# Kernel tuning notes

Measured on AMD Instinct MI355X. Metric: run time of the kernel, lower is better.

The kernel has to match this reference:

```python
import jax, jax.numpy as jnp
import numpy as np

B, T, W, H = 4, 4096, 1024, 8
BW = W // H  # block width


@jax.custom_vjp
def sqrt_bound(x):
    return jnp.sqrt(x)

def _sb_fwd(x):
    return jnp.sqrt(x), x

def _sb_bwd(x, g):
    return (g / jnp.sqrt(jnp.clip(4.0 * x, 1e-6)),)

sqrt_bound.defvjp(_sb_fwd, _sb_bwd)


def block_diag_linear(x, w, b):
    # x: [B,T,W] -> [B,T,H,BW]; w: [H,BW,BW]; b: [H,BW]
    xb = x.reshape(x.shape[0], x.shape[1], H, BW)
    y = jnp.einsum('bthi,hij->bthj', xb, w) + b
    return y.reshape(x.shape)


def setup_inputs() -> dict:
    key = jax.random.key(0)
    k1, k2, k3, k4 = jax.random.split(key, 4)
    x = jax.random.normal(k1, (B, T, W), dtype=jnp.float32)
    segment_pos = jnp.broadcast_to(jnp.arange(T, dtype=jnp.int32)[None, :], (B, T))
    std = 1.0 / np.sqrt(BW)
    w_in = std * jax.random.normal(k2, (H, BW, BW), dtype=jnp.float32)
    b_in = jnp.zeros((H, BW), dtype=jnp.float32)
    w_a = std * jax.random.normal(k3, (H, BW, BW), dtype=jnp.float32)
    b_a = jnp.zeros((H, BW), dtype=jnp.float32)
    # rnn_param_init: a_param = log(u^{-0.5} - 1), u ~ U(min_rad^2+eps, max_rad^2+eps)
    u = jax.random.uniform(k4, (W,), dtype=jnp.float32,
                           minval=0.9 ** 2 + 1e-8, maxval=0.999 ** 2 + 1e-8)
    a_param = jnp.log(jnp.exp(-0.5 * jnp.log(u)) - 1.0)
    return {'x': x, 'segment_pos': segment_pos, 'a_param': a_param,
            'w_in': w_in, 'b_in': b_in, 'w_a': w_a, 'b_a': b_a}


def reference(x, segment_pos, a_param, w_in, b_in, w_a, b_a):
    gate_x = jax.nn.sigmoid(block_diag_linear(x, w_in, b_in))
    gate_a = jax.nn.sigmoid(block_diag_linear(x, w_a, b_a))
    log_a = -8.0 * gate_a * jax.nn.softplus(a_param)  # [B,T,W]
    a = jnp.exp(log_a)
    multiplier = sqrt_bound(1.0 - jnp.exp(2.0 * log_a))
    normed_x = x * gate_x * multiplier
    reset = (segment_pos == 0)  # [B,T] bool
    a_eff = a * (~reset)[..., None].astype(a.dtype)
    # diagonal linear recurrence h_t = a_t * h_{t-1} + x_t via lax.scan over time
    def step(h, inp):
        a_t, x_t = inp
        h = a_t * h + x_t
        return h, h
    xs = (jnp.swapaxes(a_eff, 0, 1), jnp.swapaxes(normed_x, 0, 1))  # [T,B,W]
    h0 = jnp.zeros((x.shape[0], x.shape[2]), dtype=x.dtype)
    _, ys = jax.lax.scan(step, h0, xs)
    return jnp.swapaxes(ys, 0, 1)  # [B,T,W]
```

## Files before the change

### kernel.cpp

```cpp
#include <hip/hip_runtime.h>
#include <math.h>

#define NB 4
#define NT 4096
#define NW 1024
#define NH 8
#define CHUNK 64
#define NCH 64
#define STRIDE_A 136

typedef __attribute__((ext_vector_type(8))) short short8;
typedef __attribute__((ext_vector_type(4))) float f32x4;

__device__ __forceinline__ short bf16rne(float f) {
    unsigned u = __float_as_uint(f);
    u += 0x7fffu + ((u >> 16) & 1u);
    return (short)(u >> 16);
}

__global__ __launch_bounds__(256)
void k0_wfrag(const float* __restrict__ w_in, const float* __restrict__ w_a,
              short* __restrict__ wfH, uint4* __restrict__ poison)
{
    int idx = blockIdx.x * 256 + threadIdx.x;
    uint4 nv; nv.x = nv.y = nv.z = nv.w = 0xFFFFFFFFu;
    poison[idx]          = nv;
    poison[idx + 65536]  = nv;
    poison[idx + 131072] = nv;

    int j4 = (idx & 31) * 4;
    int i  = (idx >> 5) & 127;
    int h  = (idx >> 12) & 7;
    int g  = idx >> 15;
    const float* w = g ? w_a : w_in;
    float4 v = *(const float4*)&w[((size_t)h * 128 + i) * 128 + j4];
    const float vf[4] = {v.x, v.y, v.z, v.w};
    const int ks = i >> 5, q = (i >> 3) & 3, jj = i & 7;
    #pragma unroll
    for (int d = 0; d < 4; ++d) {
        int j = j4 + d;
        int lane = q * 16 + (j & 15);
        int ntg = j >> 4;
        size_t dst = ((size_t)(((h * 2 + g) * 4 + ks) * 8 + ntg) * 64 + lane) * 8 + jj;
        wfH[dst] = bf16rne(vf[d]);
    }
}

__global__ __launch_bounds__(512)
void k_fused(const float* __restrict__ x, const int* __restrict__ seg,
             const float* __restrict__ a_param,
             const float* __restrict__ b_in, const float* __restrict__ b_a,
             const short* __restrict__ wfH,
             float* __restrict__ Ag, float* __restrict__ Hg,
             float* __restrict__ Hi, float* __restrict__ out)
{
    __shared__ short sA[64 * STRIDE_A];

    const int h   = blockIdx.x;
    const int bc  = blockIdx.y;
    const int b   = bc >> 6, c = bc & 63;
    const int tid = threadIdx.x;
    const int wave = tid >> 6, lane = tid & 63;
    const int quad = lane >> 4, m = lane & 15;
    const int row0 = b * NT + c * CHUNK;

    {
        const int r  = tid >> 3;
        const int k0 = (tid & 7) * 16;
        const float4* px = (const float4*)(x + (size_t)(row0 + r) * NW + h * 128 + k0);
        float4 v0 = px[0], v1 = px[1], v2 = px[2], v3 = px[3];
        const float f[16] = {v0.x, v0.y, v0.z, v0.w, v1.x, v1.y, v1.z, v1.w,
                             v2.x, v2.y, v2.z, v2.w, v3.x, v3.y, v3.z, v3.w};
        short8 s0, s1;
        #pragma unroll
        for (int j = 0; j < 8; ++j) { s0[j] = bf16rne(f[j]); s1[j] = bf16rne(f[8 + j]); }
        *(short8*)&sA[r * STRIDE_A + k0]     = s0;
        *(short8*)&sA[r * STRIDE_A + k0 + 8] = s1;
    }
    __syncthreads();

    f32x4 acc[2][4];
    #pragma unroll
    for (int g = 0; g < 2; ++g)
        #pragma unroll
        for (int mt = 0; mt < 4; ++mt)
            acc[g][mt] = (f32x4){0.f, 0.f, 0.f, 0.f};

    #pragma unroll
    for (int ks = 0; ks < 4; ++ks) {
        short8 ah[4];
        #pragma unroll
        for (int mt = 0; mt < 4; ++mt)
            ah[mt] = *(const short8*)&sA[(mt * 16 + m) * STRIDE_A + ks * 32 + quad * 8];
        #pragma unroll
        for (int g = 0; g < 2; ++g) {
            const size_t fo = ((size_t)(((h * 2 + g) * 4 + ks) * 8 + wave) * 64 + lane) * 8;
            short8 bh = *(const short8*)(wfH + fo);
            #pragma unroll
            for (int mt = 0; mt < 4; ++mt)
                acc[g][mt] = __builtin_amdgcn_mfma_f32_16x16x32_bf16(ah[mt], bh, acc[g][mt], 0, 0, 0);
        }
    }

    const int col  = wave * 16 + m;
    const int colg = h * 128 + col;
    const float bi = b_in[colg];
    const float ba = b_a[colg];
    const float c2 = -8.0f * log1pf(expf(a_param[colg]));

    float cA = 1.f, cH = 0.f;
    float Pf[4][4], Hf[4][4];
    #pragma unroll
    for (int mt = 0; mt < 4; ++mt) {
        float lP[4], lH[4];
        {
            float xv[4]; int sv[4];
            #pragma unroll
            for (int r = 0; r < 4; ++r) {
                const int rowi = row0 + mt * 16 + quad * 4 + r;
                xv[r] = x[(size_t)rowi * NW + colg];
                sv[r] = seg[rowi];
            }
            #pragma unroll
            for (int r = 0; r < 4; ++r) {
                const float zx = acc[0][mt][r] + bi;
                const float za = acc[1][mt][r] + ba;
                const float gx = __fdividef(1.f, 1.f + __expf(-zx));
                const float ga = __fdividef(1.f, 1.f + __expf(-za));
                const float a  = __expf(c2 * ga);
                const float mult = sqrtf(fmaxf(fmaf(-a, a, 1.f), 0.f));
                const float av = (sv[r] == 0) ? 0.f : a;
                const float nx = xv[r] * gx * mult;
                lP[r] = (r == 0) ? av : lP[r - 1] * av;
                lH[r] = (r == 0) ? nx : fmaf(av, lH[r - 1], nx);
            }
        }
        float iA = lP[3], iH = lH[3];
        float uA = __shfl_up(iA, 16), uH = __shfl_up(iH, 16);
        if (quad >= 1) { iH = fmaf(iA, uH, iH); iA = uA * iA; }
        uA = __shfl_up(iA, 32); uH = __shfl_up(iH, 32);
        if (quad >= 2) { iH = fmaf(iA, uH, iH); iA = uA * iA; }
        float eA = __shfl_up(iA, 16), eH = __shfl_up(iH, 16);
        if (quad == 0) { eA = 1.f; eH = 0.f; }
        const float mAt = __shfl(iA, 48 + m);
        const float mHt = __shfl(iH, 48 + m);
        const float pA = cA * eA;
        const float pH = fmaf(eA, cH, eH);
        cH = fmaf(mAt, cH, mHt);
        cA = cA * mAt;
        #pragma unroll
        for (int r = 0; r < 4; ++r) {
            Pf[mt][r] = pA * lP[r];
            Hf[mt][r] = fmaf(lP[r], pH, lH[r]);
        }
    }

    const size_t cb0 = (size_t)(h * NB + b) * NCH * 128;
    float hp = 0.f;
    if (quad == 0) {
        const size_t oc = cb0 + (size_t)c * 128 + col;
        if (c > 0) {
            __hip_atomic_store(&Ag[oc], cA, __ATOMIC_RELAXED, __HIP_MEMORY_SCOPE_AGENT);
            __hip_atomic_store(&Hg[oc], cH, __ATOMIC_RELAXED, __HIP_MEMORY_SCOPE_AGENT);
            float accA = 1.f, accH = 0.f;
            int k = c - 1;
            for (;;) {
                const size_t o = cb0 + (size_t)k * 128 + col;
                const float hv = __hip_atomic_load(&Hi[o], __ATOMIC_RELAXED, __HIP_MEMORY_SCOPE_AGENT);
                const float A_ = __hip_atomic_load(&Ag[o], __ATOMIC_RELAXED, __HIP_MEMORY_SCOPE_AGENT);
                const float H_ = __hip_atomic_load(&Hg[o], __ATOMIC_RELAXED, __HIP_MEMORY_SCOPE_AGENT);
                if (!__builtin_isnan(hv)) {
                    hp = fmaf(accA, hv, accH);
                    break;
                }
                if (__builtin_isnan(A_) || __builtin_isnan(H_)) {
                    __builtin_amdgcn_s_sleep(2);
                    continue;
                }
                accH = fmaf(accA, H_, accH);
                accA *= A_;
                --k;
            }
        }
        __hip_atomic_store(&Hi[oc], fmaf(cA, hp, cH), __ATOMIC_RELAXED, __HIP_MEMORY_SCOPE_AGENT);
    }
    hp = __shfl(hp, m);

    #pragma unroll
    for (int mt = 0; mt < 4; ++mt) {
        #pragma unroll
        for (int r = 0; r < 4; ++r) {
            const int rowi = row0 + mt * 16 + quad * 4 + r;
            out[(size_t)rowi * NW + colg] = fmaf(Pf[mt][r], hp, Hf[mt][r]);
        }
    }
}

extern "C" void kernel_launch(void* const* d_in, const int* in_sizes, int n_in,
                              void* d_out, int out_size, void* d_ws, size_t ws_size,
                              hipStream_t stream)
{
    (void)in_sizes; (void)n_in; (void)out_size; (void)ws_size;
    const float* x    = (const float*)d_in[0];
    const int*   seg  = (const int*)  d_in[1];
    const float* ap   = (const float*)d_in[2];
    const float* w_in = (const float*)d_in[3];
    const float* b_in = (const float*)d_in[4];
    const float* w_a  = (const float*)d_in[5];
    const float* b_a  = (const float*)d_in[6];
    float* out = (float*)d_out;

    const size_t NTOP = (size_t)NH * NB * NCH * 128;
    float* Ag  = (float*)d_ws;
    float* Hg  = Ag + NTOP;
    float* Hi  = Hg + NTOP;
    short* wfH = (short*)(Hi + NTOP);

    k0_wfrag<<<256, 256, 0, stream>>>(w_in, w_a, wfH, (uint4*)Ag);
    dim3 g1(NH, NB * NCH);
    k_fused<<<g1, 512, 0, stream>>>(x, seg, ap, b_in, b_a, wfH, Ag, Hg, Hi, out);
}
```

Baseline: 159.9 us.

## Double chunk length and replace serial lookback with packed parallel 32-chunk lookback

Each block now handles 128 timesteps in two 64-row MFMA halves, which halves the number of chunks per sequence. The inter-chunk carry protocol packs the chunk aggregates A and H into one 64-bit atomic word and drops the separate inclusive-prefix array. All four quads of a wave poll up to 8 predecessors each in parallel and combine the results with shuffles. The aim is a shorter cross-block dependency chain and fewer atomic round-trips. The cost is higher register pressure (launch bounds of 512 threads with 4 blocks) and every block now reading all predecessor aggregates instead of stopping at the first ready inclusive prefix.

```diff
diff --git a/kernel.cpp b/kernel.cpp
--- a/kernel.cpp
+++ b/kernel.cpp
@@ -5,12 +5,13 @@
 #define NT 4096
 #define NW 1024
 #define NH 8
-#define CHUNK 64
-#define NCH 64
+#define CHUNK 128
+#define NCH 32
 #define STRIDE_A 136
 
 typedef __attribute__((ext_vector_type(8))) short short8;
 typedef __attribute__((ext_vector_type(4))) float f32x4;
+typedef unsigned long long u64;
 
 __device__ __forceinline__ short bf16rne(float f) {
     unsigned u = __float_as_uint(f);
@@ -24,9 +25,7 @@
 {
     int idx = blockIdx.x * 256 + threadIdx.x;
     uint4 nv; nv.x = nv.y = nv.z = nv.w = 0xFFFFFFFFu;
-    poison[idx]          = nv;
-    poison[idx + 65536]  = nv;
-    poison[idx + 131072] = nv;
+    poison[idx] = nv;
 
     int j4 = (idx & 31) * 4;
     int i  = (idx >> 5) & 127;
@@ -46,19 +45,18 @@
     }
 }
 
-__global__ __launch_bounds__(512)
+__global__ __launch_bounds__(512, 4)
 void k_fused(const float* __restrict__ x, const int* __restrict__ seg,
              const float* __restrict__ a_param,
              const float* __restrict__ b_in, const float* __restrict__ b_a,
              const short* __restrict__ wfH,
-             float* __restrict__ Ag, float* __restrict__ Hg,
-             float* __restrict__ Hi, float* __restrict__ out)
+             float2* __restrict__ AGH, float* __restrict__ out)
 {
-    __shared__ short sA[64 * STRIDE_A];
+    __shared__ short sA[CHUNK * STRIDE_A];
 
     const int h   = blockIdx.x;
     const int bc  = blockIdx.y;
-    const int b   = bc >> 6, c = bc & 63;
+    const int b   = bc >> 5, c = bc & 31;
     const int tid = threadIdx.x;
     const int wave = tid >> 6, lane = tid & 63;
     const int quad = lane >> 4, m = lane & 15;
@@ -67,40 +65,21 @@
     {
         const int r  = tid >> 3;
         const int k0 = (tid & 7) * 16;
-        const float4* px = (const float4*)(x + (size_t)(row0 + r) * NW + h * 128 + k0);
-        float4 v0 = px[0], v1 = px[1], v2 = px[2], v3 = px[3];
-        const float f[16] = {v0.x, v0.y, v0.z, v0.w, v1.x, v1.y, v1.z, v1.w,
-                             v2.x, v2.y, v2.z, v2.w, v3.x, v3.y, v3.z, v3.w};
-        short8 s0, s1;
-        #pragma unroll
-        for (int j = 0; j < 8; ++j) { s0[j] = bf16rne(f[j]); s1[j] = bf16rne(f[8 + j]); }
-        *(short8*)&sA[r * STRIDE_A + k0]     = s0;
-        *(short8*)&sA[r * STRIDE_A + k0 + 8] = s1;
+        #pragma unroll
+        for (int hh = 0; hh < 2; ++hh) {
+            const int rr = r + hh * 64;
+            const float4* px = (const float4*)(x + (size_t)(row0 + rr) * NW + h * 128 + k0);
+            float4 v0 = px[0], v1 = px[1], v2 = px[2], v3 = px[3];
+            const float f[16] = {v0.x, v0.y, v0.z, v0.w, v1.x, v1.y, v1.z, v1.w,
+                                 v2.x, v2.y, v2.z, v2.w, v3.x, v3.y, v3.z, v3.w};
+            short8 s0, s1;
+            #pragma unroll
+            for (int j = 0; j < 8; ++j) { s0[j] = bf16rne(f[j]); s1[j] = bf16rne(f[8 + j]); }
+            *(short8*)&sA[rr * STRIDE_A + k0]     = s0;
+            *(short8*)&sA[rr * STRIDE_A + k0 + 8] = s1;
+        }
     }
     __syncthreads();
-
-    f32x4 acc[2][4];
-    #pragma unroll
-    for (int g = 0; g < 2; ++g)
-        #pragma unroll
-        for (int mt = 0; mt < 4; ++mt)
-            acc[g][mt] = (f32x4){0.f, 0.f, 0.f, 0.f};
-
-    #pragma unroll
-    for (int ks = 0; ks < 4; ++ks) {
-        short8 ah[4];
-        #pragma unroll
-        for (int mt = 0; mt < 4; ++mt)
-            ah[mt] = *(const short8*)&sA[(mt * 16 + m) * STRIDE_A + ks * 32 + quad * 8];
-        #pragma unroll
-        for (int g = 0; g < 2; ++g) {
-            const size_t fo = ((size_t)(((h * 2 + g) * 4 + ks) * 8 + wave) * 64 + lane) * 8;
-            short8 bh = *(const short8*)(wfH + fo);
-            #pragma unroll
-            for (int mt = 0; mt < 4; ++mt)
-                acc[g][mt] = __builtin_amdgcn_mfma_f32_16x16x32_bf16(ah[mt], bh, acc[g][mt], 0, 0, 0);
-        }
-    }
 
     const int col  = wave * 16 + m;
     const int colg = h * 128 + col;
@@ -109,91 +88,134 @@
     const float c2 = -8.0f * log1pf(expf(a_param[colg]));
 
     float cA = 1.f, cH = 0.f;
-    float Pf[4][4], Hf[4][4];
+    float Pf[8][4], Hf[8][4];
     #pragma unroll
-    for (int mt = 0; mt < 4; ++mt) {
-        float lP[4], lH[4];
-        {
-            float xv[4]; int sv[4];
+    for (int hh = 0; hh < 2; ++hh) {
+        f32x4 acc[2][4];
+        #pragma unroll
+        for (int g = 0; g < 2; ++g)
+            #pragma unroll
+            for (int mt = 0; mt < 4; ++mt)
+                acc[g][mt] = (f32x4){0.f, 0.f, 0.f, 0.f};
+
+        #pragma unroll
+        for (int ks = 0; ks < 4; ++ks) {
+            short8 ah[4];
+            #pragma unroll
+            for (int mt = 0; mt < 4; ++mt)
+                ah[mt] = *(const short8*)&sA[(hh * 64 + mt * 16 + m) * STRIDE_A + ks * 32 + quad * 8];
+            #pragma unroll
+            for (int g = 0; g < 2; ++g) {
+                const size_t fo = ((size_t)(((h * 2 + g) * 4 + ks) * 8 + wave) * 64 + lane) * 8;
+                short8 bh = *(const short8*)(wfH + fo);
+                #pragma unroll
+                for (int mt = 0; mt < 4; ++mt)
+                    acc[g][mt] = __builtin_amdgcn_mfma_f32_16x16x32_bf16(ah[mt], bh, acc[g][mt], 0, 0, 0);
+            }
+        }
+
+        #pragma unroll
+        for (int mt = 0; mt < 4; ++mt) {
+            float lP[4], lH[4];
+            {
+                float xv[4]; int sv[4];
+                #pragma unroll
+                for (int r = 0; r < 4; ++r) {
+                    const int rowi = row0 + hh * 64 + mt * 16 + quad * 4 + r;
+                    xv[r] = x[(size_t)rowi * NW + colg];
+                    sv[r] = seg[rowi];
+                }
+                #pragma unroll
+                for (int r = 0; r < 4; ++r) {
+                    const float zx = acc[0][mt][r] + bi;
+                    const float za = acc[1][mt][r] + ba;
+                    const float gx = __fdividef(1.f, 1.f + __expf(-zx));
+                    const float ga = __fdividef(1.f, 1.f + __expf(-za));
+                    const float a  = __expf(c2 * ga);
+                    const float mult = sqrtf(fmaxf(fmaf(-a, a, 1.f), 0.f));
+                    const float av = (sv[r] == 0) ? 0.f : a;
+                    const float nx = xv[r] * gx * mult;
+                    lP[r] = (r == 0) ? av : lP[r - 1] * av;
+                    lH[r] = (r == 0) ? nx : fmaf(av, lH[r - 1], nx);
+                }
+            }
+            float iA = lP[3], iH = lH[3];
+            float uA = __shfl_up(iA, 16), uH = __shfl_up(iH, 16);
+            if (quad >= 1) { iH = fmaf(iA, uH, iH); iA = uA * iA; }
+            uA = __shfl_up(iA, 32); uH = __shfl_up(iH, 32);
+            if (quad >= 2) { iH = fmaf(iA, uH, iH); iA = uA * iA; }
+            float eA = __shfl_up(iA, 16), eH = __shfl_up(iH, 16);
+            if (quad == 0) { eA = 1.f; eH = 0.f; }
+            const float mAt = __shfl(iA, 48 + m);
+            const float mHt = __shfl(iH, 48 + m);
+            const float pA = cA * eA;
+            const float pH = fmaf(eA, cH, eH);
+            cH = fmaf(mAt, cH, mHt);
+            cA = cA * mAt;
             #pragma unroll
             for (int r = 0; r < 4; ++r) {
-                const int rowi = row0 + mt * 16 + quad * 4 + r;
-                xv[r] = x[(size_t)rowi * NW + colg];
-                sv[r] = seg[rowi];
-            }
+                Pf[hh * 4 + mt][r] = pA * lP[r];
+                Hf[hh * 4 + mt][r] = fmaf(lP[r], pH, lH[r]);
+            }
+        }
+    }
+
+    const size_t cb0 = (size_t)(h * NB + b) * NCH * 128;
+    if (quad == 0) {
+        const u64 pk = ((u64)__float_as_uint(cH) << 32) | (u64)__float_as_uint(cA);
+        __hip_atomic_store((u64*)&AGH[cb0 + (size_t)c * 128 + col], pk,
+                           __ATOMIC_RELAXED, __HIP_MEMORY_SCOPE_AGENT);
+    }
+
+    float hp = 0.f;
+    {
+        const int base = c - 1 - quad * 8;
+        const int nj   = base < 0 ? 0 : (base >= 7 ? 8 : base + 1);
+        float a_ = 1.f, h_ = 0.f;
+        if (nj > 0) {
+            int folded = 0;
+            for (;;) {
+                u64 pk[8];
+                #pragma unroll
+                for (int j = 0; j < 8; ++j) {
+                    int idx = base - j; idx = idx < 0 ? 0 : idx;
+                    pk[j] = __hip_atomic_load((const u64*)&AGH[cb0 + (size_t)idx * 128 + col],
+                                              __ATOMIC_RELAXED, __HIP_MEMORY_SCOPE_AGENT);
+                }
+                bool stall = false;
+                #pragma unroll
+                for (int j = 0; j < 8; ++j) {
+                    if (j < folded || j >= nj || stall) continue;
+                    const float A_ = __uint_as_float((unsigned)pk[j]);
+                    if (__builtin_isnan(A_)) { stall = true; continue; }
+                    const float H_ = __uint_as_float((unsigned)(pk[j] >> 32));
+                    h_ = fmaf(a_, H_, h_);
+                    a_ *= A_;
+                    folded = j + 1;
+                }
+                if (folded >= nj) break;
+                __builtin_amdgcn_s_sleep(1);
+            }
+        }
+        float accA = 1.f;
+        #pragma unroll
+        for (int q = 0; q < 4; ++q) {
+            const float Aq = __shfl(a_, q * 16 + m);
+            const float Hq = __shfl(h_, q * 16 + m);
+            hp = fmaf(accA, Hq, hp);
+            accA *= Aq;
+        }
+    }
+
+    #pragma unroll
+    for (int hh = 0; hh < 2; ++hh)
+        #pragma unroll
+        for (int mt = 0; mt < 4; ++mt)
             #pragma unroll
             for (int r = 0; r < 4; ++r) {
-                const float zx = acc[0][mt][r] + bi;
-                const float za = acc[1][mt][r] + ba;
-                const float gx = __fdividef(1.f, 1.f + __expf(-zx));
-                const float ga = __fdividef(1.f, 1.f + __expf(-za));
-                const float a  = __expf(c2 * ga);
-                const float mult = sqrtf(fmaxf(fmaf(-a, a, 1.f), 0.f));
-                const float av = (sv[r] == 0) ? 0.f : a;
-                const float nx = xv[r] * gx * mult;
-                lP[r] = (r == 0) ? av : lP[r - 1] * av;
-                lH[r] = (r == 0) ? nx : fmaf(av, lH[r - 1], nx);
-            }
-        }
-        float iA = lP[3], iH = lH[3];
-        float uA = __shfl_up(iA, 16), uH = __shfl_up(iH, 16);
-        if (quad >= 1) { iH = fmaf(iA, uH, iH); iA = uA * iA; }
-        uA = __shfl_up(iA, 32); uH = __shfl_up(iH, 32);
-        if (quad >= 2) { iH = fmaf(iA, uH, iH); iA = uA * iA; }
-        float eA = __shfl_up(iA, 16), eH = __shfl_up(iH, 16);
-        if (quad == 0) { eA = 1.f; eH = 0.f; }
-        const float mAt = __shfl(iA, 48 + m);
-        const float mHt = __shfl(iH, 48 + m);
-        const float pA = cA * eA;
-        const float pH = fmaf(eA, cH, eH);
-        cH = fmaf(mAt, cH, mHt);
-        cA = cA * mAt;
-        #pragma unroll
-        for (int r = 0; r < 4; ++r) {
-            Pf[mt][r] = pA * lP[r];
-            Hf[mt][r] = fmaf(lP[r], pH, lH[r]);
-        }
-    }
-
-    const size_t cb0 = (size_t)(h * NB + b) * NCH * 128;
-    float hp = 0.f;
-    if (quad == 0) {
-        const size_t oc = cb0 + (size_t)c * 128 + col;
-        if (c > 0) {
-            __hip_atomic_store(&Ag[oc], cA, __ATOMIC_RELAXED, __HIP_MEMORY_SCOPE_AGENT);
-            __hip_atomic_store(&Hg[oc], cH, __ATOMIC_RELAXED, __HIP_MEMORY_SCOPE_AGENT);
-            float accA = 1.f, accH = 0.f;
-            int k = c - 1;
-            for (;;) {
-                const size_t o = cb0 + (size_t)k * 128 + col;
-                const float hv = __hip_atomic_load(&Hi[o], __ATOMIC_RELAXED, __HIP_MEMORY_SCOPE_AGENT);
-                const float A_ = __hip_atomic_load(&Ag[o], __ATOMIC_RELAXED, __HIP_MEMORY_SCOPE_AGENT);
-                const float H_ = __hip_atomic_load(&Hg[o], __ATOMIC_RELAXED, __HIP_MEMORY_SCOPE_AGENT);
-                if (!__builtin_isnan(hv)) {
-                    hp = fmaf(accA, hv, accH);
-                    break;
-                }
-                if (__builtin_isnan(A_) || __builtin_isnan(H_)) {
-                    __builtin_amdgcn_s_sleep(2);
-                    continue;
-                }
-                accH = fmaf(accA, H_, accH);
-                accA *= A_;
-                --k;
-            }
-        }
-        __hip_atomic_store(&Hi[oc], fmaf(cA, hp, cH), __ATOMIC_RELAXED, __HIP_MEMORY_SCOPE_AGENT);
-    }
-    hp = __shfl(hp, m);
-
-    #pragma unroll
-    for (int mt = 0; mt < 4; ++mt) {
-        #pragma unroll
-        for (int r = 0; r < 4; ++r) {
-            const int rowi = row0 + mt * 16 + quad * 4 + r;
-            out[(size_t)rowi * NW + colg] = fmaf(Pf[mt][r], hp, Hf[mt][r]);
-        }
-    }
+                const int rowi = row0 + hh * 64 + mt * 16 + quad * 4 + r;
+                out[(size_t)rowi * NW + colg] = fmaf(Pf[hh * 4 + mt][r], hp, Hf[hh * 4 + mt][r]);
+            }
 }
 
 extern "C" void kernel_launch(void* const* d_in, const int* in_sizes, int n_in,
@@ -211,12 +233,10 @@
     float* out = (float*)d_out;
 
     const size_t NTOP = (size_t)NH * NB * NCH * 128;
-    float* Ag  = (float*)d_ws;
-    float* Hg  = Ag + NTOP;
-    float* Hi  = Hg + NTOP;
-    short* wfH = (short*)(Hi + NTOP);
-
-    k0_wfrag<<<256, 256, 0, stream>>>(w_in, w_a, wfH, (uint4*)Ag);
+    float2* AGH = (float2*)d_ws;
+    short*  wfH = (short*)(AGH + NTOP);
+
+    k0_wfrag<<<256, 256, 0, stream>>>(w_in, w_a, wfH, (uint4*)AGH);
     dim3 g1(NH, NB * NCH);
-    k_fused<<<g1, 512, 0, stream>>>(x, seg, ap, b_in, b_a, wfH, Ag, Hg, Hi, out);
-}
+    k_fused<<<g1, 512, 0, stream>>>(x, seg, ap, b_in, b_a, wfH, AGH, out);
+}
```

Result: slower. 205.0 us (+28.2%).
